# Performance work log

Measured on AMD Instinct MI355X. Metric: run time of the kernel, lower is better.

Reference implementation:

```python
import jax, jax.numpy as jnp
import numpy as np

D_MODEL = 1024
N_HEADS = 16
D_K = D_MODEL // N_HEADS
B, S = 2, 2048


def setup_inputs() -> dict:
    key = jax.random.key(0)
    ks = jax.random.split(key, 5)
    sc = 1.0 / np.sqrt(D_MODEL)
    return {
        "x": jax.random.normal(ks[0], (B, S, D_MODEL), dtype=jnp.float32),
        "W_qkv": jax.random.normal(ks[1], (D_MODEL, 3 * D_MODEL), dtype=jnp.float32) * sc,
        "b_qkv": jnp.zeros((3 * D_MODEL,), dtype=jnp.float32),
        "W_out": jax.random.normal(ks[2], (D_MODEL, D_MODEL), dtype=jnp.float32) * sc,
        "b_out": jnp.zeros((D_MODEL,), dtype=jnp.float32),
    }


def reference(x, W_qkv, b_qkv, W_out, b_out):
    Bb, Ss, _ = x.shape
    qkv = x @ W_qkv + b_qkv                     # [B,S,3*D]
    qkv = qkv.reshape(Bb, Ss, 3, N_HEADS, D_K)
    qkv = jnp.transpose(qkv, (2, 0, 3, 1, 4))   # [3,B,H,S,Dk]
    q, k, v = qkv[0], qkv[1], qkv[2]
    scale = jnp.asarray(np.sqrt(D_K), dtype=x.dtype)
    attn = jnp.einsum('bhsd,bhtd->bhst', q, k) / scale  # [B,H,S,S]
    attn = jax.nn.softmax(attn, axis=-1)
    out = jnp.einsum('bhst,bhtd->bhsd', attn, v)        # [B,H,S,Dk]
    out = jnp.transpose(out, (0, 2, 1, 3)).reshape(Bb, Ss, D_MODEL)
    return out @ W_out + b_out
```

## Files before the change

### kernel.cpp

```cpp
#include <hip/hip_runtime.h>

typedef __bf16 bf16x8 __attribute__((ext_vector_type(8)));
typedef __bf16 bf16x4 __attribute__((ext_vector_type(4)));
typedef __bf16 bf16x2 __attribute__((ext_vector_type(2)));
typedef float f32x4 __attribute__((ext_vector_type(4)));
typedef unsigned short u16;
typedef unsigned short u16x4 __attribute__((ext_vector_type(4)));
typedef unsigned short u16x8 __attribute__((ext_vector_type(8)));
typedef unsigned int u32;
typedef unsigned int u32x2 __attribute__((ext_vector_type(2)));
typedef unsigned int u32x4 __attribute__((ext_vector_type(4)));

__device__ __forceinline__ u16 f2bu(float f) {
  __bf16 h = (__bf16)f;
  return __builtin_bit_cast(u16, h);
}

__device__ __forceinline__ void gld16(const u16* g, const __bf16* lds) {
  __builtin_amdgcn_global_load_lds(
      (const __attribute__((address_space(1))) u32*)(uintptr_t)g,
      (__attribute__((address_space(3))) u32*)(u32)(uintptr_t)lds, 16, 0, 0);
}

__device__ __forceinline__ void tr_tile(const float* __restrict__ in, u16* __restrict__ out,
                                        int R, int C, int bx, int by, int tid) {
  __shared__ u16 t[64][65];
  int tx = tid & 63, ty = tid >> 6;
  int r0 = by * 64, c0 = bx * 64;
  for (int i = 0; i < 16; ++i)
    t[ty + i * 4][tx] = f2bu(in[(size_t)(r0 + ty + i * 4) * C + c0 + tx]);
  __syncthreads();
  for (int i = 0; i < 16; ++i)
    out[(size_t)(c0 + ty + i * 4) * R + r0 + tx] = t[tx][ty + i * 4];
}

__global__ __launch_bounds__(256) void prep(const float* __restrict__ Wqkv,
                                            u16* __restrict__ Wqkv_t,
                                            const float* __restrict__ Wout,
                                            u16* __restrict__ Wout_t,
                                            const float* __restrict__ x,
                                            u16* __restrict__ xb) {
  int id = blockIdx.x, tid = threadIdx.x;
  if (id < 768) {
    tr_tile(Wqkv, Wqkv_t, 1024, 3072, id % 48, id / 48, tid);
  } else if (id < 1024) {
    int id2 = id - 768;
    tr_tile(Wout, Wout_t, 1024, 1024, id2 % 16, id2 / 16, tid);
  } else {
    size_t i = ((size_t)(id - 1024) * 256 + tid) * 8;
    f32x4 a0 = *(const f32x4*)(x + i);
    f32x4 a1 = *(const f32x4*)(x + i + 4);
    bf16x8 v;
    for (int j = 0; j < 4; ++j) { v[j] = (__bf16)a0[j]; v[j + 4] = (__bf16)a1[j]; }
    *(bf16x8*)(xb + i) = v;
  }
}

template <int MODE, int TM, int TN, int MT, int NT, int XM, int XN>
__global__ __launch_bounds__(256) void gemm_bt(const u16* __restrict__ A,
                                               const u16* __restrict__ Bt,
                                               const float* __restrict__ bias,
                                               void* __restrict__ O0v,
                                               u16* __restrict__ O1,
                                               u16* __restrict__ O2,
                                               int M, int N, int K) {
  constexpr int NI = TM / 32;
  constexpr int NJ = TN / 32;
  constexpr int AE = TM * 32;
  constexpr int BE = TN * 32;
  __shared__ __bf16 smem[2 * (AE + BE)];

  int tid = threadIdx.x;
  int w = tid >> 6, lane = tid & 63, quad = lane >> 4, l16 = lane & 15;
  int wr = w >> 1, wc = w & 1;

  int id = blockIdx.x;
  int xcd = id & 7, s0i = id >> 3;
  int mg = xcd % (MT / XM), ng = xcd / (MT / XM);
  int sm = s0i % XM, sn = s0i / XM;
  int m0 = (mg * XM + sm) * TM, n0 = (ng * XN + sn) * TN;

  int srow = w * 16 + (lane >> 2);
  int sch = (lane & 3) ^ ((lane >> 3) & 3);
  const u16* Ag = A + (size_t)(m0 + srow) * K + sch * 8;
  const u16* Bg = Bt + (size_t)(n0 + srow) * K + sch * 8;

  int swl = (quad ^ ((l16 >> 1) & 3)) << 3;

  f32x4 acc[NI][NJ] = {};

#define GLD_STEP(c, kk)                                                          \
  {                                                                              \
    for (int p = 0; p < TM / 64; ++p)                                            \
      gld16(Ag + (size_t)p * 64 * K + (kk), smem + (c) * (AE + BE) + w * 512 + p * 2048); \
    for (int p = 0; p < TN / 64; ++p)                                            \
      gld16(Bg + (size_t)p * 64 * K + (kk), smem + (c) * (AE + BE) + AE + w * 512 + p * 2048); \
  }

  GLD_STEP(0, 0);
  int NS = K / 32;
  for (int s = 0; s < NS; ++s) {
    int cur = s & 1;
    __syncthreads();
    if (s + 1 < NS) GLD_STEP(1 - cur, (s + 1) * 32);
    const __bf16* Asub = smem + cur * (AE + BE);
    const __bf16* Bsub = Asub + AE;
    bf16x8 af[NI], bfr[NJ];
    for (int i = 0; i < NI; ++i)
      af[i] = *(const bf16x8*)(Asub + (wr * (TM / 2) + i * 16 + l16) * 32 + swl);
    for (int j = 0; j < NJ; ++j)
      bfr[j] = *(const bf16x8*)(Bsub + (wc * (TN / 2) + j * 16 + l16) * 32 + swl);
    for (int i = 0; i < NI; ++i)
      for (int j = 0; j < NJ; ++j)
        acc[i][j] = __builtin_amdgcn_mfma_f32_16x16x32_bf16(af[i], bfr[j], acc[i][j], 0, 0, 0);
  }
#undef GLD_STEP

  if (MODE == 0) {
    float* O0 = (float*)O0v;
    for (int j = 0; j < NJ; ++j) {
      int n = n0 + wc * (TN / 2) + j * 16 + l16;
      float bv = bias[n];
      for (int i = 0; i < NI; ++i) {
        int mb = m0 + wr * (TM / 2) + i * 16 + quad * 4;
        for (int r = 0; r < 4; ++r)
          O0[(size_t)(mb + r) * N + n] = acc[i][j][r] + bv;
      }
    }
  } else {
    constexpr float QSC = 0.125f * 1.44269504f;
    int bw = n0 >> 10;
    if (bw < 2) {
      u16* Od = bw ? O1 : (u16*)O0v;
      float sc = bw ? 1.f : QSC;
      for (int j = 0; j < NJ; ++j) {
        int n = n0 + wc * (TN / 2) + j * 16 + l16;
        int h = (n & 1023) >> 6, d = n & 63;
        float bv = bias[n];
        for (int i = 0; i < NI; ++i) {
          int m = m0 + wr * (TM / 2) + i * 16 + quad * 4;
          int b = m >> 11, s = m & 2047;
          for (int r = 0; r < 4; ++r)
            Od[(((size_t)(b * 16 + h)) * 2048 + (s + r)) * 64 + d] = f2bu((acc[i][j][r] + bv) * sc);
        }
      }
    } else {
      __syncthreads();
      u16* Lt = (u16*)smem;
      for (int j = 0; j < NJ; ++j) {
        int col = wc * (TN / 2) + j * 16 + l16;
        float bv = bias[n0 + col];
        for (int i = 0; i < NI; ++i) {
          int m_ = wr * (TM / 2) + i * 16 + quad * 4;
          u16x4 val;
          for (int r = 0; r < 4; ++r) val[r] = f2bu(acc[i][j][r] + bv);
          int g = (m_ >> 2) ^ (col & 15);
          *(u16x4*)(Lt + (size_t)col * TM + g * 4) = val;
        }
      }
      __syncthreads();
      int b = m0 >> 11, s0 = m0 & 2047;
      for (int k = 0; k < TM * TN / 8 / 256; ++k) {
        int ch = tid + k * 256;
        int col = ch >> 4, s8 = (ch & 15) * 8;
        int g0 = ((s8 >> 2) + 0) ^ (col & 15);
        int g1 = ((s8 >> 2) + 1) ^ (col & 15);
        u16x4 lo = *(const u16x4*)(Lt + (size_t)col * TM + g0 * 4);
        u16x4 hi = *(const u16x4*)(Lt + (size_t)col * TM + g1 * 4);
        u16x8 v8;
        for (int z = 0; z < 4; ++z) { v8[z] = lo[z]; v8[4 + z] = hi[z]; }
        int n = n0 + col;
        int h = (n & 1023) >> 6, d = n & 63;
        *(u16x8*)(O2 + (((size_t)(b * 16 + h)) * 64 + d) * 2048 + s0 + s8) = v8;
      }
    }
  }
}

__global__ __launch_bounds__(512, 4) void flash_attn(const u16* __restrict__ Q,
                                                     const u16* __restrict__ K,
                                                     const u16* __restrict__ Vt,
                                                     u16* __restrict__ AO) {
  constexpr int S = 2048;
  constexpr int HALF = S / 2;
  constexpr int NIT = HALF / 64;
  __shared__ __bf16 lds[2][2][2][64 * 64];

  int bh = blockIdx.x, qbase = blockIdx.y * 128;
  int tid = threadIdx.x;
  int grp = tid >> 8, gtid = tid & 255;
  int w = gtid >> 6, lane = tid & 63, quad = lane >> 4, l16 = lane & 15;

  const u16* Qh = Q + (size_t)bh * S * 64;
  const u16* Kh = K + (size_t)bh * S * 64 + (size_t)grp * HALF * 64;
  const u16* Vh = Vt + (size_t)bh * 64 * S + grp * HALF;

  int qrowA = qbase + w * 32 + l16;
  int qrowB = qrowA + 16;
  bf16x8 qf0a = *(const bf16x8*)(Qh + (size_t)qrowA * 64 + quad * 8);
  bf16x8 qf1a = *(const bf16x8*)(Qh + (size_t)qrowA * 64 + 32 + quad * 8);
  bf16x8 qf0b = *(const bf16x8*)(Qh + (size_t)qrowB * 64 + quad * 8);
  bf16x8 qf1b = *(const bf16x8*)(Qh + (size_t)qrowB * 64 + 32 + quad * 8);

  bf16x8 vone;
#pragma unroll
  for (int j = 0; j < 8; ++j) vone[j] = (__bf16)1.0f;

  int r0s = gtid >> 3, b0s = gtid & 7;
  int r1s = r0s + 32;
  int ko0 = r0s * 64 + ((b0s ^ (r0s & 7)) << 3);
  int ko1 = r1s * 64 + ((b0s ^ (r1s & 7)) << 3);

  __bf16* Ks0 = &lds[grp][0][0][0];
  __bf16* Vs0 = &lds[grp][1][0][0];

  bf16x8 kr0, kr1, vr0, vr1;
#define LOAD_TILE(tb)                                                   \
  {                                                                     \
    kr0 = *(const bf16x8*)(Kh + (size_t)((tb) + r0s) * 64 + b0s * 8);   \
    kr1 = *(const bf16x8*)(Kh + (size_t)((tb) + r1s) * 64 + b0s * 8);   \
    vr0 = *(const bf16x8*)(Vh + (size_t)r0s * S + (tb) + b0s * 8);      \
    vr1 = *(const bf16x8*)(Vh + (size_t)r1s * S + (tb) + b0s * 8);      \
  }
#define STORE_TILE(c)                                                   \
  {                                                                     \
    *(bf16x8*)(Ks0 + (c) * 4096 + ko0) = kr0;                           \
    *(bf16x8*)(Ks0 + (c) * 4096 + ko1) = kr1;                           \
    *(bf16x8*)(Vs0 + (c) * 4096 + ko0) = vr0;                           \
    *(bf16x8*)(Vs0 + (c) * 4096 + ko1) = vr1;                           \
  }

  LOAD_TILE(0);
  STORE_TILE(0);
  LOAD_TILE(64);
  __syncthreads();

  f32x4 oA[4] = {};
  f32x4 oB[4] = {};
  f32x4 lfA = {};
  f32x4 lfB = {};
  int xr = l16 & 7;

  for (int it = 0; it < NIT; ++it) {
    int c = it & 1;
    if (it + 1 < NIT) STORE_TILE(1 - c);
    if (it + 2 < NIT) LOAD_TILE((it + 2) * 64);

    u32 pwA[4][2], pwB[4][2];
#pragma unroll
    for (int nt = 0; nt < 4; ++nt) {
      const __bf16* kb = Ks0 + c * 4096 + (nt * 16 + l16) * 64;
      bf16x8 kf0 = *(const bf16x8*)(kb + ((quad ^ xr) << 3));
      bf16x8 kf1 = *(const bf16x8*)(kb + (((quad + 4) ^ xr) << 3));
      f32x4 ca = {0.f, 0.f, 0.f, 0.f};
      f32x4 cb = {0.f, 0.f, 0.f, 0.f};
      ca = __builtin_amdgcn_mfma_f32_16x16x32_bf16(kf0, qf0a, ca, 0, 0, 0);
      cb = __builtin_amdgcn_mfma_f32_16x16x32_bf16(kf0, qf0b, cb, 0, 0, 0);
      ca = __builtin_amdgcn_mfma_f32_16x16x32_bf16(kf1, qf1a, ca, 0, 0, 0);
      cb = __builtin_amdgcn_mfma_f32_16x16x32_bf16(kf1, qf1b, cb, 0, 0, 0);
      bf16x2 a01 = {(__bf16)__builtin_amdgcn_exp2f(ca[0]), (__bf16)__builtin_amdgcn_exp2f(ca[1])};
      bf16x2 a23 = {(__bf16)__builtin_amdgcn_exp2f(ca[2]), (__bf16)__builtin_amdgcn_exp2f(ca[3])};
      bf16x2 b01 = {(__bf16)__builtin_amdgcn_exp2f(cb[0]), (__bf16)__builtin_amdgcn_exp2f(cb[1])};
      bf16x2 b23 = {(__bf16)__builtin_amdgcn_exp2f(cb[2]), (__bf16)__builtin_amdgcn_exp2f(cb[3])};
      pwA[nt][0] = __builtin_bit_cast(u32, a01);
      pwA[nt][1] = __builtin_bit_cast(u32, a23);
      pwB[nt][0] = __builtin_bit_cast(u32, b01);
      pwB[nt][1] = __builtin_bit_cast(u32, b23);
    }

    bf16x8 pfA[2], pfB[2];
#pragma unroll
    for (int h = 0; h < 2; ++h) {
      u32 GA[2], HA[2], GB[2], HB[2];
#pragma unroll
      for (int w2 = 0; w2 < 2; ++w2) {
        u32x2 s1a = __builtin_amdgcn_permlane32_swap(pwA[2 * h][w2], pwA[2 * h + 1][w2], false, false);
        u32x2 s2a = __builtin_amdgcn_permlane16_swap(s1a[0], s1a[1], false, false);
        GA[w2] = s2a[0];
        HA[w2] = s2a[1];
        u32x2 s1b = __builtin_amdgcn_permlane32_swap(pwB[2 * h][w2], pwB[2 * h + 1][w2], false, false);
        u32x2 s2b = __builtin_amdgcn_permlane16_swap(s1b[0], s1b[1], false, false);
        GB[w2] = s2b[0];
        HB[w2] = s2b[1];
      }
      u32x4 pa = {GA[0], GA[1], HA[0], HA[1]};
      u32x4 pb = {GB[0], GB[1], HB[0], HB[1]};
      pfA[h] = __builtin_bit_cast(bf16x8, pa);
      pfB[h] = __builtin_bit_cast(bf16x8, pb);
    }

    lfA = __builtin_amdgcn_mfma_f32_16x16x32_bf16(pfA[0], vone, lfA, 0, 0, 0);
    lfA = __builtin_amdgcn_mfma_f32_16x16x32_bf16(pfA[1], vone, lfA, 0, 0, 0);
    lfB = __builtin_amdgcn_mfma_f32_16x16x32_bf16(pfB[0], vone, lfB, 0, 0, 0);
    lfB = __builtin_amdgcn_mfma_f32_16x16x32_bf16(pfB[1], vone, lfB, 0, 0, 0);

#pragma unroll
    for (int dt = 0; dt < 4; ++dt) {
      const __bf16* vb = Vs0 + c * 4096 + (dt * 16 + l16) * 64;
      bf16x8 v0 = *(const bf16x8*)(vb + ((quad ^ xr) << 3));
      bf16x8 v1 = *(const bf16x8*)(vb + (((quad + 4) ^ xr) << 3));
      oA[dt] = __builtin_amdgcn_mfma_f32_16x16x32_bf16(pfA[0], v0, oA[dt], 0, 0, 0);
      oB[dt] = __builtin_amdgcn_mfma_f32_16x16x32_bf16(pfB[0], v0, oB[dt], 0, 0, 0);
      oA[dt] = __builtin_amdgcn_mfma_f32_16x16x32_bf16(pfA[1], v1, oA[dt], 0, 0, 0);
      oB[dt] = __builtin_amdgcn_mfma_f32_16x16x32_bf16(pfB[1], v1, oB[dt], 0, 0, 0);
    }
    __syncthreads();
  }
#undef LOAD_TILE
#undef STORE_TILE

  float* mf = (float*)&lds[0][0][0][0];
  if (grp) {
    float* p = mf + (size_t)gtid * 41;
#pragma unroll
    for (int dt = 0; dt < 4; ++dt)
#pragma unroll
      for (int r = 0; r < 4; ++r) {
        p[dt * 4 + r] = oA[dt][r];
        p[16 + dt * 4 + r] = oB[dt][r];
      }
#pragma unroll
    for (int r = 0; r < 4; ++r) {
      p[32 + r] = lfA[r];
      p[36 + r] = lfB[r];
    }
  }
  __syncthreads();
  if (!grp) {
    const float* p = mf + (size_t)gtid * 41;
    float linvA[4], linvB[4];
#pragma unroll
    for (int r = 0; r < 4; ++r) {
      linvA[r] = 1.f / (lfA[r] + p[32 + r]);
      linvB[r] = 1.f / (lfB[r] + p[36 + r]);
    }
    int b = bh >> 4, h = bh & 15;
    for (int dt = 0; dt < 4; ++dt)
      for (int r = 0; r < 4; ++r) {
        int sA = qbase + w * 32 + quad * 4 + r;
        int sB = sA + 16;
        int d = dt * 16 + l16;
        AO[(((size_t)b * 2048 + sA) * 16 + h) * 64 + d] = f2bu((oA[dt][r] + p[dt * 4 + r]) * linvA[r]);
        AO[(((size_t)b * 2048 + sB) * 16 + h) * 64 + d] = f2bu((oB[dt][r] + p[16 + dt * 4 + r]) * linvB[r]);
      }
  }
}

extern "C" void kernel_launch(void* const* d_in, const int* in_sizes, int n_in,
                              void* d_out, int out_size, void* d_ws, size_t ws_size,
                              hipStream_t stream) {
  const float* x    = (const float*)d_in[0];
  const float* Wqkv = (const float*)d_in[1];
  const float* bqkv = (const float*)d_in[2];
  const float* Wout = (const float*)d_in[3];
  const float* bout = (const float*)d_in[4];
  float* out = (float*)d_out;

  u16* ws = (u16*)d_ws;
  size_t off = 0;
  u16* Wqkv_t = ws + off; off += (size_t)3072 * 1024;
  u16* Wout_t = ws + off; off += (size_t)1024 * 1024;
  u16* xb     = ws + off; off += (size_t)4096 * 1024;
  u16* Qb     = ws + off; off += (size_t)32 * 2048 * 64;
  u16* Kb     = ws + off; off += (size_t)32 * 2048 * 64;
  u16* Vtb    = ws + off; off += (size_t)32 * 2048 * 64;
  u16* AO     = xb;

  prep<<<dim3(3072), 256, 0, stream>>>(Wqkv, Wqkv_t, Wout, Wout_t, x, xb);
  gemm_bt<1, 128, 128, 32, 24, 8, 12><<<dim3(768), 256, 0, stream>>>(
      xb, Wqkv_t, bqkv, (void*)Qb, Kb, Vtb, 4096, 3072, 1024);
  flash_attn<<<dim3(32, 16), 512, 0, stream>>>(Qb, Kb, Vtb, AO);
  gemm_bt<0, 128, 64, 32, 16, 8, 8><<<dim3(512), 256, 0, stream>>>(
      AO, Wout_t, bout, (void*)out, nullptr, nullptr, 4096, 1024, 1024);
}
```

Before: 176.6 us.

## Stage K/V tiles with direct global-to-LDS loads and raise MFMA wave priority

```diff
diff --git a/kernel.cpp b/kernel.cpp
--- a/kernel.cpp
+++ b/kernel.cpp
@@ -206,33 +206,25 @@
 #pragma unroll
   for (int j = 0; j < 8; ++j) vone[j] = (__bf16)1.0f;
 
-  int r0s = gtid >> 3, b0s = gtid & 7;
-  int r1s = r0s + 32;
-  int ko0 = r0s * 64 + ((b0s ^ (r0s & 7)) << 3);
-  int ko1 = r1s * 64 + ((b0s ^ (r1s & 7)) << 3);
-
   __bf16* Ks0 = &lds[grp][0][0][0];
   __bf16* Vs0 = &lds[grp][1][0][0];
 
-  bf16x8 kr0, kr1, vr0, vr1;
-#define LOAD_TILE(tb)                                                   \
+  int lrow = lane >> 3, lgr = lane & 7;
+  int sgr = (lgr ^ lrow) << 3;
+  const u16* Ksrc = Kh + ((size_t)(w * 16) + lrow) * 64 + sgr;
+  const u16* Vsrc = Vh + ((size_t)(w * 16) + lrow) * S + sgr;
+  const __bf16* Kdst = Ks0 + w * 16 * 64;
+  const __bf16* Vdst = Vs0 + w * 16 * 64;
+
+#define STAGE(c, tb)                                                    \
   {                                                                     \
-    kr0 = *(const bf16x8*)(Kh + (size_t)((tb) + r0s) * 64 + b0s * 8);   \
-    kr1 = *(const bf16x8*)(Kh + (size_t)((tb) + r1s) * 64 + b0s * 8);   \
-    vr0 = *(const bf16x8*)(Vh + (size_t)r0s * S + (tb) + b0s * 8);      \
-    vr1 = *(const bf16x8*)(Vh + (size_t)r1s * S + (tb) + b0s * 8);      \
-  }
-#define STORE_TILE(c)                                                   \
-  {                                                                     \
-    *(bf16x8*)(Ks0 + (c) * 4096 + ko0) = kr0;                           \
-    *(bf16x8*)(Ks0 + (c) * 4096 + ko1) = kr1;                           \
-    *(bf16x8*)(Vs0 + (c) * 4096 + ko0) = vr0;                           \
-    *(bf16x8*)(Vs0 + (c) * 4096 + ko1) = vr1;                           \
-  }
-
-  LOAD_TILE(0);
-  STORE_TILE(0);
-  LOAD_TILE(64);
+    gld16(Ksrc + (size_t)(tb) * 64, Kdst + (c) * 4096);                 \
+    gld16(Ksrc + (size_t)((tb) + 8) * 64, Kdst + (c) * 4096 + 512);     \
+    gld16(Vsrc + (tb), Vdst + (c) * 4096);                              \
+    gld16(Vsrc + (size_t)8 * S + (tb), Vdst + (c) * 4096 + 512);        \
+  }
+
+  STAGE(0, 0);
   __syncthreads();
 
   f32x4 oA[4] = {};
@@ -243,8 +235,7 @@
 
   for (int it = 0; it < NIT; ++it) {
     int c = it & 1;
-    if (it + 1 < NIT) STORE_TILE(1 - c);
-    if (it + 2 < NIT) LOAD_TILE((it + 2) * 64);
+    if (it + 1 < NIT) STAGE(1 - c, (it + 1) * 64);
 
     u32 pwA[4][2], pwB[4][2];
 #pragma unroll
@@ -254,10 +245,12 @@
       bf16x8 kf1 = *(const bf16x8*)(kb + (((quad + 4) ^ xr) << 3));
       f32x4 ca = {0.f, 0.f, 0.f, 0.f};
       f32x4 cb = {0.f, 0.f, 0.f, 0.f};
+      __builtin_amdgcn_s_setprio(1);
       ca = __builtin_amdgcn_mfma_f32_16x16x32_bf16(kf0, qf0a, ca, 0, 0, 0);
       cb = __builtin_amdgcn_mfma_f32_16x16x32_bf16(kf0, qf0b, cb, 0, 0, 0);
       ca = __builtin_amdgcn_mfma_f32_16x16x32_bf16(kf1, qf1a, ca, 0, 0, 0);
       cb = __builtin_amdgcn_mfma_f32_16x16x32_bf16(kf1, qf1b, cb, 0, 0, 0);
+      __builtin_amdgcn_s_setprio(0);
       bf16x2 a01 = {(__bf16)__builtin_amdgcn_exp2f(ca[0]), (__bf16)__builtin_amdgcn_exp2f(ca[1])};
       bf16x2 a23 = {(__bf16)__builtin_amdgcn_exp2f(ca[2]), (__bf16)__builtin_amdgcn_exp2f(ca[3])};
       bf16x2 b01 = {(__bf16)__builtin_amdgcn_exp2f(cb[0]), (__bf16)__builtin_amdgcn_exp2f(cb[1])};
@@ -289,25 +282,28 @@
       pfB[h] = __builtin_bit_cast(bf16x8, pb);
     }
 
+    __builtin_amdgcn_s_setprio(1);
     lfA = __builtin_amdgcn_mfma_f32_16x16x32_bf16(pfA[0], vone, lfA, 0, 0, 0);
     lfA = __builtin_amdgcn_mfma_f32_16x16x32_bf16(pfA[1], vone, lfA, 0, 0, 0);
     lfB = __builtin_amdgcn_mfma_f32_16x16x32_bf16(pfB[0], vone, lfB, 0, 0, 0);
     lfB = __builtin_amdgcn_mfma_f32_16x16x32_bf16(pfB[1], vone, lfB, 0, 0, 0);
+    __builtin_amdgcn_s_setprio(0);
 
 #pragma unroll
     for (int dt = 0; dt < 4; ++dt) {
       const __bf16* vb = Vs0 + c * 4096 + (dt * 16 + l16) * 64;
       bf16x8 v0 = *(const bf16x8*)(vb + ((quad ^ xr) << 3));
       bf16x8 v1 = *(const bf16x8*)(vb + (((quad + 4) ^ xr) << 3));
+      __builtin_amdgcn_s_setprio(1);
       oA[dt] = __builtin_amdgcn_mfma_f32_16x16x32_bf16(pfA[0], v0, oA[dt], 0, 0, 0);
       oB[dt] = __builtin_amdgcn_mfma_f32_16x16x32_bf16(pfB[0], v0, oB[dt], 0, 0, 0);
       oA[dt] = __builtin_amdgcn_mfma_f32_16x16x32_bf16(pfA[1], v1, oA[dt], 0, 0, 0);
       oB[dt] = __builtin_amdgcn_mfma_f32_16x16x32_bf16(pfB[1], v1, oB[dt], 0, 0, 0);
+      __builtin_amdgcn_s_setprio(0);
     }
     __syncthreads();
   }
-#undef LOAD_TILE
-#undef STORE_TILE
+#undef STAGE
 
   float* mf = (float*)&lds[0][0][0][0];
   if (grp) {
```

Result: no change. 173.8 us (-1.6%).
